# Performance work log

Measured on AMD Instinct MI355X. Metric: run time of the kernel, lower is better.

The kernel has to match this reference:

```python
import jax, jax.numpy as jnp
import numpy as np

N_AGENTS = 8; N_HEADS = 4; HYP = 128; EMB = 32; ENT_DIM = 64
BS = 64; T = 64; NE = 32


def setup_inputs() -> dict:
    key = jax.random.key(0)
    ks = jax.random.split(key, 8)
    p = lambda k, shape: jax.random.normal(k, shape, dtype=jnp.float32) * 0.1
    return {
        "agent_qs": jax.random.normal(ks[0], (BS, T, N_AGENTS), dtype=jnp.float32),
        "entities": jax.random.normal(ks[1], (BS, T, NE, ENT_DIM), dtype=jnp.float32),
        "entity_mask": jax.random.randint(ks[2], (BS, T, NE), 0, 2, dtype=jnp.int32),
        "fc1_w": p(ks[3], (4, HYP, ENT_DIM)), "fc1_b": jnp.zeros((4, HYP), jnp.float32),
        "qkv_w": p(ks[4], (4, 3 * HYP, HYP)), "qkv_b": jnp.zeros((4, 3 * HYP), jnp.float32),
        "out_w": p(ks[5], (4, HYP, HYP)), "out_b": jnp.zeros((4, HYP), jnp.float32),
        "fc2_w": p(ks[6], (4, EMB, HYP)), "fc2_b": jnp.zeros((4, EMB), jnp.float32),
    }


def _hypernet(entities, emask, fc1_w, fc1_b, qkv_w, qkv_b, out_w, out_b, fc2_w, fc2_b):
    # entities: [B, ne, ed]; emask: [B, ne] int (1 = entity absent)
    B, ne, _ = entities.shape
    hd = HYP // N_HEADS
    x1 = jax.nn.relu(jnp.einsum('bne,he->bnh', entities, fc1_w) + fc1_b)  # [B, ne, HYP]
    agent_mask = emask[:, :N_AGENTS]                                      # [B, na]
    # attn_mask = 1 - (1-agent_mask) x (1-entity_mask); nonzero => masked out
    attn_mask = 1.0 - (1.0 - agent_mask.astype(jnp.float32))[:, :, None] * \
                      (1.0 - emask.astype(jnp.float32))[:, None, :]       # [B, na, ne]
    qkv = jnp.einsum('bnh,gh->bng', x1, qkv_w) + qkv_b                    # [B, ne, 3*HYP]
    q, k, v = jnp.split(qkv, 3, axis=-1)
    q = q[:, :N_AGENTS].reshape(B, N_AGENTS, N_HEADS, hd).transpose(0, 2, 1, 3)
    k = k.reshape(B, ne, N_HEADS, hd).transpose(0, 2, 1, 3)
    v = v.reshape(B, ne, N_HEADS, hd).transpose(0, 2, 1, 3)
    logits = jnp.einsum('bhqd,bhkd->bhqk', q, k) / jnp.sqrt(jnp.float32(hd))
    masked = attn_mask[:, None] > 0                                       # [B, 1, na, ne]
    logits = jnp.where(masked, -1e9, logits)
    w = jax.nn.softmax(logits, axis=-1)
    # rows fully masked -> zero weights (matches nan-fill in torch impl)
    w = jnp.where(jnp.all(masked, axis=-1, keepdims=True), 0.0, w)
    attn = jnp.einsum('bhqk,bhkd->bhqd', w, v).transpose(0, 2, 1, 3).reshape(B, N_AGENTS, HYP)
    x2 = jnp.einsum('bnh,oh->bno', attn, out_w) + out_b
    x2 = jnp.where(agent_mask[:, :, None] > 0, 0.0, x2)                   # post_mask
    x3 = jnp.einsum('bnh,eh->bne', x2, fc2_w) + fc2_b
    x3 = jnp.where(agent_mask[:, :, None] > 0, 0.0, x3)                   # masked_fill
    return x3  # [B, n_agents, EMB]


def reference(agent_qs, entities, entity_mask, fc1_w, fc1_b, qkv_w, qkv_b, out_w, out_b, fc2_w, fc2_b):
    bs, t, ne, ed = entities.shape
    ents = entities.reshape(bs * t, ne, ed)
    emask = entity_mask.reshape(bs * t, ne)
    qs = agent_qs.reshape(bs * t, 1, N_AGENTS)
    # vmap over the 4 stacked hypernets (w1, b1, w_final, V)
    outs = jax.vmap(_hypernet, in_axes=(None, None, 0, 0, 0, 0, 0, 0, 0, 0))(
        ents, emask, fc1_w, fc1_b, qkv_w, qkv_b, out_w, out_b, fc2_w, fc2_b)
    w1 = jax.nn.softmax(outs[0], axis=-1)            # matrix mode: [B, na, EMB]
    b1 = outs[1].mean(axis=1)[:, None, :]            # vector mode: [B, 1, EMB]
    wf = outs[2].mean(axis=1)[:, :, None]            # vector mode: [B, EMB, 1]
    wf = jax.nn.softmax(wf, axis=-1)                 # softmax over size-1 dim (faithful)
    v = outs[3].mean(axis=(1, 2))[:, None, None]     # scalar mode: [B, 1, 1]
    hidden = jnp.einsum('bqa,bae->bqe', qs, w1) + b1
    y = jnp.einsum('bqe,bek->bqk', hidden, wf) + v
    return y.reshape(bs, t, 1)
```

## Files before the change

kernel.cpp:

```cpp
#include <hip/hip_runtime.h>
#include <math.h>

#define BPB 4
#define NBLK 1024
#define SCALE 0.17677669529663687f

typedef short short8 __attribute__((ext_vector_type(8)));
typedef float f32x4 __attribute__((ext_vector_type(4)));

__device__ __forceinline__ unsigned short f2bf(float x) {
  unsigned int u = __float_as_uint(x);
  u += 0x7fffu + ((u >> 16) & 1u);
  return (unsigned short)(u >> 16);
}
__device__ __forceinline__ unsigned pk2(float a, float b) {
  return (unsigned)f2bf(a) | ((unsigned)f2bf(b) << 16);
}
__device__ __forceinline__ float bf2f(unsigned int lo16) {
  return __uint_as_float(lo16 << 16);
}
__device__ __forceinline__ int tile_addr(int r, int k) {
  int g = k >> 3;
  int p = (g ^ ((r >> 1) & 3)) & 3;
  return r * 32 + p * 8 + (k & 7);
}
__device__ __forceinline__ int rm_addr(int r, int k) {
  int g = k >> 3;
  int r3 = r & 7;
  int rot = ((r3 << 2) | (r3 >> 1)) & 7;
  int p = (g & 8) | ((g & 7) ^ rot);
  return r * 128 + p * 8 + (k & 7);
}

__global__ void prep(const float* __restrict__ fc1_w, const float* __restrict__ qkv_w,
                     const float* __restrict__ qkv_b, const float* __restrict__ out_w,
                     const float* __restrict__ out_b, const float* __restrict__ fc2_w,
                     const float* __restrict__ fc2_b,
                     unsigned short* __restrict__ wbf, float* __restrict__ wsf) {
  const int blk = blockIdx.x;
  const int t = threadIdx.x;
  __shared__ float cw[128], ow2[128], red[128];
  if (blk < 40) {
    int o = blk * 256 + t;
    const float* src;
    int dst;
    if (o < 2048) {
      int gi = o >> 10, rem = o & 1023, n = rem >> 3, kg = rem & 7;
      int g = gi ? 3 : 1;
      src = fc1_w + ((g << 7) + n) * 64 + kg * 8;
      int lane = (kg & 3) * 16 + (n & 15);
      int f = (n >> 4) * 2 + (kg >> 2);
      dst = ((gi * 16 + f) * 64 + lane) * 8;
    } else if (o < 6144) {
      int o2 = o - 2048;
      int gi = o2 >> 11, rem = o2 & 2047, n = rem >> 4, kg = rem & 15;
      int g = gi ? 3 : 1;
      src = qkv_w + ((g * 384 + 128 + n) << 7) + kg * 8;
      int lane = (kg & 3) * 16 + (n & 15);
      int f = (n >> 4) * 4 + (kg >> 2);
      dst = 16384 + ((gi * 32 + f) * 64 + lane) * 8;
    } else {
      int o2 = o - 6144;
      int gi = o2 >> 11, rem = o2 & 2047, n = rem >> 4, kg = rem & 15;
      int g = gi ? 3 : 1;
      src = qkv_w + ((g * 384 + n) << 7) + kg * 8;
      int lane = (kg & 3) * 16 + (n & 15);
      int f = (n >> 4) * 4 + (kg >> 2);
      dst = 49152 + ((gi * 32 + f) * 64 + lane) * 8;
    }
    float4 v0 = *(const float4*)src;
    float4 v1 = *(const float4*)(src + 4);
    uint4 p;
    p.x = pk2(v0.x, v0.y); p.y = pk2(v0.z, v0.w);
    p.z = pk2(v1.x, v1.y); p.w = pk2(v1.z, v1.w);
    *(uint4*)&wbf[dst] = p;
  } else {
    const int gi = blk - 40;
    const int g = gi ? 3 : 1;
    if (t < 128) {
      const float* fw = fc2_w + g * 32 * 128;
      float s = 0.f;
      for (int e = 0; e < 32; ++e) s += fw[e * 128 + t];
      cw[t] = s;
    }
    __syncthreads();
    if (t < 128) {
      const float* ow = out_w + g * 128 * 128;
      float s = 0.f;
      for (int h = 0; h < 128; ++h) s += ow[h * 128 + t] * cw[h];
      ow2[t] = s;
    }
    __syncthreads();
    float* wsg = wsf + gi * 1024;
    const float* qwv = qkv_w + (size_t)(g * 3 + 2) * 128 * 128;
    for (int o = t; o < 512; o += 256) {
      int hh = o >> 7, h2 = o & 127;
      float s = 0.f;
      for (int d = 0; d < 32; ++d) s += qwv[(hh * 32 + d) * 128 + h2] * ow2[hh * 32 + d];
      wsg[o] = s;
    }
    if (t < 4) {
      const float* qbv = qkv_b + g * 384 + 256;
      float s = 0.f;
      for (int d = 0; d < 32; ++d) s += qbv[t * 32 + d] * ow2[t * 32 + d];
      wsg[512 + t] = s;
    }
    if (t < 128) {
      float x = out_b[g * 128 + t] * cw[t];
      if (t < 32) x += fc2_b[g * 32 + t];
      red[t] = x;
    }
    __syncthreads();
    if (t < 64) {
      float s = red[t] + red[t + 64];
      for (int o = 32; o; o >>= 1) s += __shfl_xor(s, o, 64);
      if (t == 0) wsg[516] = s;
    }
  }
}

__global__ __launch_bounds__(512, 4)
void mixer(const float* __restrict__ agent_qs,
           const float* __restrict__ entities,
           const int* __restrict__ emask,
           const float* __restrict__ fc1_b,
           const float* __restrict__ qkv_b,
           const unsigned short* __restrict__ wbf,
           const float* __restrict__ wsf,
           float* __restrict__ out) {
  __shared__ __align__(16) unsigned short sEK[16384];
  __shared__ __align__(16) unsigned short sX1[16384];
  __shared__ __align__(16) unsigned short sQ[4096];
  __shared__ __align__(16) float sVW[1024];
  __shared__ float sVP[BPB][4][32];
  __shared__ int sMm[128];
  __shared__ float sS[8];

  const int t = threadIdx.x;
  const int lane = t & 63;
  const int w = t >> 6;
  const int r = lane & 15, kg = lane >> 4;
  const int bb0 = blockIdx.x * BPB;

  if (t < 128) sMm[t] = emask[bb0 * 32 + t];

  const short8* W1f = (const short8*)wbf;
  const short8* Wkf = (const short8*)(wbf + 16384);
  const short8* Wqf = (const short8*)(wbf + 49152);

  float wreg[4][2][4];

  for (int gi = 0; gi < 2; ++gi) {
    const int g = gi ? 3 : 1;
    {
      const float4* Eg = (const float4*)entities + (size_t)bb0 * 512;
#pragma unroll
      for (int i = 0; i < 4; ++i) {
        int f4 = i * 512 + t;
        float4 v = Eg[f4];
        int k4 = f4 & 15, e = (f4 >> 4) & 31, bbi = f4 >> 9;
        int k = k4 * 4;
        int addr = bbi * 2048 + ((e >> 4) * 2 + (k >> 5)) * 512 + tile_addr(e & 15, k & 31);
        uint2 pkv;
        pkv.x = pk2(v.x, v.y);
        pkv.y = pk2(v.z, v.w);
        *(uint2*)&sEK[addr] = pkv;
      }
      if (t < 256) ((float4*)sVW)[t] = ((const float4*)(wsf + gi * 1024))[t];
    }
    __syncthreads();
    {
      const int b = w >> 1, mtl = w & 1;
      f32x4 acc[8];
#pragma unroll
      for (int nt = 0; nt < 8; ++nt) acc[nt] = {0.f, 0.f, 0.f, 0.f};
#pragma unroll
      for (int kc = 0; kc < 2; ++kc) {
        short8 ef = *(const short8*)&sEK[b * 2048 + (mtl * 2 + kc) * 512 + tile_addr(r, kg * 8)];
#pragma unroll
        for (int nt = 0; nt < 8; ++nt)
          acc[nt] = __builtin_amdgcn_mfma_f32_16x16x32_bf16(
              W1f[(gi * 16 + nt * 2 + kc) * 64 + lane], ef, acc[nt], 0, 0, 0);
      }
      const float* b1 = fc1_b + g * 128;
#pragma unroll
      for (int nt = 0; nt < 8; ++nt) {
        int hbase = nt * 16 + kg * 4;
        float4 bb4 = *(const float4*)&b1[hbase];
        float v0 = fmaxf(acc[nt][0] + bb4.x, 0.f);
        float v1 = fmaxf(acc[nt][1] + bb4.y, 0.f);
        float v2 = fmaxf(acc[nt][2] + bb4.z, 0.f);
        float v3 = fmaxf(acc[nt][3] + bb4.w, 0.f);
        uint2 pkv;
        pkv.x = pk2(v0, v1);
        pkv.y = pk2(v2, v3);
        *(uint2*)&sX1[b * 4096 + (mtl * 4 + (hbase >> 5)) * 512 + tile_addr(r, hbase & 31)] = pkv;
      }
    }
    __syncthreads();
    {
      const int b = w >> 1, mtl = w & 1;
      f32x4 acc[8];
#pragma unroll
      for (int nt = 0; nt < 8; ++nt) acc[nt] = {0.f, 0.f, 0.f, 0.f};
#pragma unroll
      for (int kc = 0; kc < 4; ++kc) {
        short8 xf = *(const short8*)&sX1[b * 4096 + (mtl * 4 + kc) * 512 + tile_addr(r, kg * 8)];
#pragma unroll
        for (int nt = 0; nt < 8; ++nt)
          acc[nt] = __builtin_amdgcn_mfma_f32_16x16x32_bf16(
              Wkf[(gi * 32 + nt * 4 + kc) * 64 + lane], xf, acc[nt], 0, 0, 0);
      }
      const float* bk = qkv_b + g * 384 + 128;
      const int ent = mtl * 16 + r;
#pragma unroll
      for (int nt = 0; nt < 8; ++nt) {
        int hbase = nt * 16 + kg * 4;
        float4 bb4 = *(const float4*)&bk[hbase];
        uint2 pkv;
        pkv.x = pk2(acc[nt][0] + bb4.x, acc[nt][1] + bb4.y);
        pkv.y = pk2(acc[nt][2] + bb4.z, acc[nt][3] + bb4.w);
        *(uint2*)&sEK[b * 4096 + rm_addr(ent, hbase)] = pkv;
      }
      const int mt = w >> 2, ntp = w & 3;
      const int b_rd = mt * 2 + (r >> 3);
      f32x4 qacc[2];
      qacc[0] = {0.f, 0.f, 0.f, 0.f};
      qacc[1] = {0.f, 0.f, 0.f, 0.f};
#pragma unroll
      for (int kc = 0; kc < 4; ++kc) {
        short8 xf = *(const short8*)&sX1[b_rd * 4096 + kc * 512 + tile_addr(r & 7, kg * 8)];
#pragma unroll
        for (int j = 0; j < 2; ++j)
          qacc[j] = __builtin_amdgcn_mfma_f32_16x16x32_bf16(
              Wqf[(gi * 32 + (ntp * 2 + j) * 4 + kc) * 64 + lane], xf, qacc[j], 0, 0, 0);
      }
      const float* bq = qkv_b + g * 384;
#pragma unroll
      for (int j = 0; j < 2; ++j) {
        int hbase = (ntp * 2 + j) * 16 + kg * 4;
        float4 bb4 = *(const float4*)&bq[hbase];
        uint2 pkv;
        pkv.x = pk2(qacc[j][0] + bb4.x, qacc[j][1] + bb4.y);
        pkv.y = pk2(qacc[j][2] + bb4.z, qacc[j][3] + bb4.w);
        *(uint2*)&sQ[(mt * 2 + (r >> 3)) * 1024 + rm_addr(r & 7, hbase)] = pkv;
      }
      const int vb = w >> 1;
      const int e = lane & 31;
      const int hh = (w & 1) * 2 + (lane >> 5);
      const int emt = e >> 4, er = e & 15;
      float a0 = sVW[512 + hh];
#pragma unroll
      for (int kc = 0; kc < 4; ++kc) {
#pragma unroll
        for (int gg = 0; gg < 4; ++gg) {
          uint4 u = *(const uint4*)&sX1[vb * 4096 + (emt * 4 + kc) * 512 + tile_addr(er, gg * 8)];
          const float* wv = &sVW[hh * 128 + kc * 32 + gg * 8];
          a0 = fmaf(bf2f(u.x & 0xffffu), wv[0], a0);
          a0 = fmaf(bf2f(u.x >> 16), wv[1], a0);
          a0 = fmaf(bf2f(u.y & 0xffffu), wv[2], a0);
          a0 = fmaf(bf2f(u.y >> 16), wv[3], a0);
          a0 = fmaf(bf2f(u.z & 0xffffu), wv[4], a0);
          a0 = fmaf(bf2f(u.z >> 16), wv[5], a0);
          a0 = fmaf(bf2f(u.w & 0xffffu), wv[6], a0);
          a0 = fmaf(bf2f(u.w >> 16), wv[7], a0);
        }
      }
      sVP[vb][hh][e] = a0;
    }
    __syncthreads();
    if (w < 4) {
      const int b = w;
      const int cl = r;
      bool ea0 = (sMm[b * 32 + cl] == 0);
      bool ea1 = (sMm[b * 32 + 16 + cl] == 0);
      bool aa[4];
#pragma unroll
      for (int reg = 0; reg < 4; ++reg) aa[reg] = (sMm[b * 32 + ((kg * 4 + reg) & 7)] == 0);
#pragma unroll
      for (int hh = 0; hh < 4; ++hh) {
        short8 af = *(const short8*)&sQ[b * 1024 + rm_addr(lane & 7, hh * 32 + kg * 8)];
        f32x4 z = {0.f, 0.f, 0.f, 0.f};
        short8 bf0 = *(const short8*)&sEK[b * 4096 + rm_addr(cl, hh * 32 + kg * 8)];
        f32x4 d0 = __builtin_amdgcn_mfma_f32_16x16x32_bf16(af, bf0, z, 0, 0, 0);
        short8 bf1 = *(const short8*)&sEK[b * 4096 + rm_addr(16 + cl, hh * 32 + kg * 8)];
        f32x4 d1 = __builtin_amdgcn_mfma_f32_16x16x32_bf16(af, bf1, z, 0, 0, 0);
#pragma unroll
        for (int reg = 0; reg < 4; ++reg) {
          float lg0 = (ea0 && aa[reg]) ? d0[reg] * SCALE : -1e30f;
          float lg1 = (ea1 && aa[reg]) ? d1[reg] * SCALE : -1e30f;
          float m = fmaxf(lg0, lg1);
          for (int o = 8; o; o >>= 1) m = fmaxf(m, __shfl_xor(m, o, 16));
          float p0 = lg0 > -1e29f ? __expf(lg0 - m) : 0.f;
          float p1 = lg1 > -1e29f ? __expf(lg1 - m) : 0.f;
          float s = p0 + p1;
          for (int o = 8; o; o >>= 1) s += __shfl_xor(s, o, 16);
          float inv = s > 0.f ? 1.f / s : 0.f;
          wreg[hh][0][reg] = p0 * inv;
          wreg[hh][1][reg] = p1 * inv;
        }
      }
      float c = 0.f;
#pragma unroll
      for (int hh = 0; hh < 4; ++hh) {
        float vp0 = sVP[b][hh][cl];
        float vp1 = sVP[b][hh][16 + cl];
        float s0 = wreg[hh][0][0] + wreg[hh][0][1] + wreg[hh][0][2] + wreg[hh][0][3];
        float s1 = wreg[hh][1][0] + wreg[hh][1][1] + wreg[hh][1][2] + wreg[hh][1][3];
        c = fmaf(vp0, s0, fmaf(vp1, s1, c));
      }
      for (int o = 16; o; o >>= 1) c += __shfl_xor(c, o, 32);
      if (lane == 0) {
        int cnt = 0;
        for (int a = 0; a < 8; ++a) cnt += (sMm[b * 32 + a] == 0);
        sS[gi * 4 + b] = c + sVW[516] * (float)cnt;
      }
    }
    __syncthreads();
  }

  if (t < BPB) {
    const float4* qs = (const float4*)(agent_qs + (size_t)(bb0 + t) * 8);
    float4 a = qs[0], b4 = qs[1];
    float q = a.x + a.y + a.z + a.w + b4.x + b4.y + b4.z + b4.w;
    out[bb0 + t] = q + sS[t] * 0.125f + sS[4 + t] * (1.f / 256.f);
  }
}

extern "C" void kernel_launch(void* const* d_in, const int* in_sizes, int n_in,
                              void* d_out, int out_size, void* d_ws, size_t ws_size,
                              hipStream_t stream) {
  const float* agent_qs = (const float*)d_in[0];
  const float* entities = (const float*)d_in[1];
  const int* emask = (const int*)d_in[2];
  const float* fc1_w = (const float*)d_in[3];
  const float* fc1_b = (const float*)d_in[4];
  const float* qkv_w = (const float*)d_in[5];
  const float* qkv_b = (const float*)d_in[6];
  const float* out_w = (const float*)d_in[7];
  const float* out_b = (const float*)d_in[8];
  const float* fc2_w = (const float*)d_in[9];
  const float* fc2_b = (const float*)d_in[10];
  float* out = (float*)d_out;
  unsigned short* wbf = (unsigned short*)d_ws;
  float* wsf = (float*)((char*)d_ws + 163840);

  prep<<<42, 256, 0, stream>>>(fc1_w, qkv_w, qkv_b, out_w, out_b, fc2_w, fc2_b, wbf, wsf);
  mixer<<<NBLK, 512, 0, stream>>>(agent_qs, entities, emask, fc1_b, qkv_b, wbf, wsf, out);
}
```

Baseline: 174.6 us.

## Fold V-projection into K MFMA tile and halve per-block batch

The collapsed value-projection vectors are packed as an extra bf16 MFMA N-tile next to the K weights, so the per-entity V reduction is done with MFMA instead of a scalar FMA loop over bf16 LDS reads. The prep kernel is split across more blocks and writes these rows plus zero padding. The mixer now handles 2 batch rows per 256-thread block instead of 4 per 512, with separate LDS buffers for E and K so entities are converted once rather than per hypernet. The V path now uses bf16 weights, which lowers its precision, and the block size and occupancy change.

```diff
diff --git a/kernel.cpp b/kernel.cpp
--- a/kernel.cpp
+++ b/kernel.cpp
@@ -1,12 +1,13 @@
 #include <hip/hip_runtime.h>
 #include <math.h>
 
-#define BPB 4
-#define NBLK 1024
+#define BPB 2
+#define NBLK 2048
 #define SCALE 0.17677669529663687f
 
 typedef short short8 __attribute__((ext_vector_type(8)));
 typedef float f32x4 __attribute__((ext_vector_type(4)));
+typedef unsigned short ushort_t;
 
 __device__ __forceinline__ unsigned short f2bf(float x) {
   unsigned int u = __float_as_uint(x);
@@ -15,9 +16,6 @@
 }
 __device__ __forceinline__ unsigned pk2(float a, float b) {
   return (unsigned)f2bf(a) | ((unsigned)f2bf(b) << 16);
-}
-__device__ __forceinline__ float bf2f(unsigned int lo16) {
-  return __uint_as_float(lo16 << 16);
 }
 __device__ __forceinline__ int tile_addr(int r, int k) {
   int g = k >> 3;
@@ -39,7 +37,7 @@
                      unsigned short* __restrict__ wbf, float* __restrict__ wsf) {
   const int blk = blockIdx.x;
   const int t = threadIdx.x;
-  __shared__ float cw[128], ow2[128], red[128];
+  __shared__ float cw[128], red[256], ow2s[32];
   if (blk < 40) {
     int o = blk * 256 + t;
     const float* src;
@@ -58,7 +56,7 @@
       src = qkv_w + ((g * 384 + 128 + n) << 7) + kg * 8;
       int lane = (kg & 3) * 16 + (n & 15);
       int f = (n >> 4) * 4 + (kg >> 2);
-      dst = 16384 + ((gi * 32 + f) * 64 + lane) * 8;
+      dst = 16384 + ((gi * 36 + f) * 64 + lane) * 8;
     } else {
       int o2 = o - 6144;
       int gi = o2 >> 11, rem = o2 & 2047, n = rem >> 4, kg = rem & 15;
@@ -66,7 +64,7 @@
       src = qkv_w + ((g * 384 + n) << 7) + kg * 8;
       int lane = (kg & 3) * 16 + (n & 15);
       int f = (n >> 4) * 4 + (kg >> 2);
-      dst = 49152 + ((gi * 32 + f) * 64 + lane) * 8;
+      dst = 53248 + ((gi * 32 + f) * 64 + lane) * 8;
     }
     float4 v0 = *(const float4*)src;
     float4 v1 = *(const float4*)(src + 4);
@@ -75,51 +73,72 @@
     p.z = pk2(v1.x, v1.y); p.w = pk2(v1.z, v1.w);
     *(uint4*)&wbf[dst] = p;
   } else {
-    const int gi = blk - 40;
+    const int mb = blk - 40;
+    const int gi = mb >> 2, hh = mb & 3;
     const int g = gi ? 3 : 1;
+    {
+      const float* fw = fc2_w + g * 4096;
+      int h2 = t & 127, half = t >> 7;
+      float s = 0.f;
+      for (int e = half * 16; e < half * 16 + 16; ++e) s += fw[e * 128 + h2];
+      red[t] = s;
+    }
+    __syncthreads();
+    if (t < 128) cw[t] = red[t] + red[t + 128];
+    __syncthreads();
+    {
+      const float* ow = out_w + g * 16384;
+      int hp = hh * 32 + (t & 31), ch = t >> 5;
+      float s = 0.f;
+      for (int h = ch * 16; h < ch * 16 + 16; ++h) s += ow[h * 128 + hp] * cw[h];
+      red[t] = s;
+    }
+    __syncthreads();
+    if (t < 32) {
+      float s = 0.f;
+      for (int c = 0; c < 8; ++c) s += red[c * 32 + t];
+      ow2s[t] = s;
+    }
+    __syncthreads();
+    {
+      const float* qwv = qkv_w + (size_t)(g * 3 + 2) * 16384;
+      int h2 = t & 127, half = t >> 7;
+      float s = 0.f;
+      for (int d = half * 16; d < half * 16 + 16; ++d)
+        s += qwv[(hh * 32 + d) * 128 + h2] * ow2s[d];
+      red[t] = s;
+    }
+    __syncthreads();
     if (t < 128) {
-      const float* fw = fc2_w + g * 32 * 128;
-      float s = 0.f;
-      for (int e = 0; e < 32; ++e) s += fw[e * 128 + t];
-      cw[t] = s;
-    }
-    __syncthreads();
-    if (t < 128) {
-      const float* ow = out_w + g * 128 * 128;
-      float s = 0.f;
-      for (int h = 0; h < 128; ++h) s += ow[h * 128 + t] * cw[h];
-      ow2[t] = s;
-    }
-    __syncthreads();
-    float* wsg = wsf + gi * 1024;
-    const float* qwv = qkv_w + (size_t)(g * 3 + 2) * 128 * 128;
-    for (int o = t; o < 512; o += 256) {
-      int hh = o >> 7, h2 = o & 127;
-      float s = 0.f;
-      for (int d = 0; d < 32; ++d) s += qwv[(hh * 32 + d) * 128 + h2] * ow2[hh * 32 + d];
-      wsg[o] = s;
-    }
-    if (t < 4) {
-      const float* qbv = qkv_b + g * 384 + 256;
-      float s = 0.f;
-      for (int d = 0; d < 32; ++d) s += qbv[t * 32 + d] * ow2[t * 32 + d];
-      wsg[512 + t] = s;
-    }
-    if (t < 128) {
-      float x = out_b[g * 128 + t] * cw[t];
-      if (t < 32) x += fc2_b[g * 32 + t];
-      red[t] = x;
-    }
-    __syncthreads();
-    if (t < 64) {
-      float s = red[t] + red[t + 64];
-      for (int o = 32; o; o >>= 1) s += __shfl_xor(s, o, 64);
-      if (t == 0) wsg[516] = s;
+      float v = red[t] + red[t + 128];
+      int k = t, kc = k >> 5, kg2 = k >> 3, j = k & 7;
+      wbf[16384 + ((gi * 36 + 32 + kc) * 64 + ((kg2 & 3) * 16 + hh)) * 8 + j] = f2bf(v);
+    }
+    if (t < 32) red[t] = qkv_b[g * 384 + 256 + hh * 32 + t] * ow2s[t];
+    __syncthreads();
+    if (t < 32) {
+      float s = red[t];
+      for (int o = 16; o; o >>= 1) s += __shfl_xor(s, o, 32);
+      if (t == 0) wsf[gi * 1024 + 512 + hh] = s;
+    }
+    if (hh == 0) {
+      for (int idx = t; idx < 1536; idx += 256) {
+        int n = 4 + (idx >> 7), k = idx & 127;
+        int kc = k >> 5, kg2 = k >> 3, j = k & 7;
+        wbf[16384 + ((gi * 36 + 32 + kc) * 64 + ((kg2 & 3) * 16 + n)) * 8 + j] = 0;
+      }
+      if (t < 128) red[t] = out_b[g * 128 + t] * cw[t] + (t < 32 ? fc2_b[g * 32 + t] : 0.f);
+      __syncthreads();
+      if (t < 64) {
+        float s = red[t] + red[t + 64];
+        for (int o = 32; o; o >>= 1) s += __shfl_xor(s, o, 64);
+        if (t == 0) wsf[gi * 1024 + 516] = s;
+      }
     }
   }
 }
 
-__global__ __launch_bounds__(512, 4)
+__global__ __launch_bounds__(256, 3)
 void mixer(const float* __restrict__ agent_qs,
            const float* __restrict__ entities,
            const int* __restrict__ emask,
@@ -128,13 +147,13 @@
            const unsigned short* __restrict__ wbf,
            const float* __restrict__ wsf,
            float* __restrict__ out) {
-  __shared__ __align__(16) unsigned short sEK[16384];
-  __shared__ __align__(16) unsigned short sX1[16384];
-  __shared__ __align__(16) unsigned short sQ[4096];
-  __shared__ __align__(16) float sVW[1024];
+  __shared__ __align__(16) ushort_t sE[4096];
+  __shared__ __align__(16) ushort_t sX1[8192];
+  __shared__ __align__(16) ushort_t sK[8192];
+  __shared__ __align__(16) ushort_t sQ[2048];
   __shared__ float sVP[BPB][4][32];
-  __shared__ int sMm[128];
-  __shared__ float sS[8];
+  __shared__ int sMm[64];
+  __shared__ float sS[4];
 
   const int t = threadIdx.x;
   const int lane = t & 63;
@@ -142,41 +161,41 @@
   const int r = lane & 15, kg = lane >> 4;
   const int bb0 = blockIdx.x * BPB;
 
-  if (t < 128) sMm[t] = emask[bb0 * 32 + t];
+  if (t < 64) sMm[t] = emask[bb0 * 32 + t];
 
   const short8* W1f = (const short8*)wbf;
-  const short8* Wkf = (const short8*)(wbf + 16384);
-  const short8* Wqf = (const short8*)(wbf + 49152);
+  const short8* Wkvf = (const short8*)(wbf + 16384);
+  const short8* Wqf = (const short8*)(wbf + 53248);
+
+  {
+    const float4* Eg = (const float4*)entities + (size_t)bb0 * 512;
+#pragma unroll
+    for (int i = 0; i < 4; ++i) {
+      int f4 = i * 256 + t;
+      float4 v = Eg[f4];
+      int k4 = f4 & 15, e = (f4 >> 4) & 31, bbi = f4 >> 9;
+      int k = k4 * 4;
+      int addr = bbi * 2048 + ((e >> 4) * 2 + (k >> 5)) * 512 + tile_addr(e & 15, k & 31);
+      uint2 pkv;
+      pkv.x = pk2(v.x, v.y);
+      pkv.y = pk2(v.z, v.w);
+      *(uint2*)&sE[addr] = pkv;
+    }
+  }
+  __syncthreads();
 
   float wreg[4][2][4];
 
   for (int gi = 0; gi < 2; ++gi) {
     const int g = gi ? 3 : 1;
     {
-      const float4* Eg = (const float4*)entities + (size_t)bb0 * 512;
-#pragma unroll
-      for (int i = 0; i < 4; ++i) {
-        int f4 = i * 512 + t;
-        float4 v = Eg[f4];
-        int k4 = f4 & 15, e = (f4 >> 4) & 31, bbi = f4 >> 9;
-        int k = k4 * 4;
-        int addr = bbi * 2048 + ((e >> 4) * 2 + (k >> 5)) * 512 + tile_addr(e & 15, k & 31);
-        uint2 pkv;
-        pkv.x = pk2(v.x, v.y);
-        pkv.y = pk2(v.z, v.w);
-        *(uint2*)&sEK[addr] = pkv;
-      }
-      if (t < 256) ((float4*)sVW)[t] = ((const float4*)(wsf + gi * 1024))[t];
-    }
-    __syncthreads();
-    {
       const int b = w >> 1, mtl = w & 1;
       f32x4 acc[8];
 #pragma unroll
       for (int nt = 0; nt < 8; ++nt) acc[nt] = {0.f, 0.f, 0.f, 0.f};
 #pragma unroll
       for (int kc = 0; kc < 2; ++kc) {
-        short8 ef = *(const short8*)&sEK[b * 2048 + (mtl * 2 + kc) * 512 + tile_addr(r, kg * 8)];
+        short8 ef = *(const short8*)&sE[b * 2048 + (mtl * 2 + kc) * 512 + tile_addr(r, kg * 8)];
 #pragma unroll
         for (int nt = 0; nt < 8; ++nt)
           acc[nt] = __builtin_amdgcn_mfma_f32_16x16x32_bf16(
@@ -200,16 +219,16 @@
     __syncthreads();
     {
       const int b = w >> 1, mtl = w & 1;
-      f32x4 acc[8];
-#pragma unroll
-      for (int nt = 0; nt < 8; ++nt) acc[nt] = {0.f, 0.f, 0.f, 0.f};
+      f32x4 acc[9];
+#pragma unroll
+      for (int nt = 0; nt < 9; ++nt) acc[nt] = {0.f, 0.f, 0.f, 0.f};
 #pragma unroll
       for (int kc = 0; kc < 4; ++kc) {
         short8 xf = *(const short8*)&sX1[b * 4096 + (mtl * 4 + kc) * 512 + tile_addr(r, kg * 8)];
 #pragma unroll
-        for (int nt = 0; nt < 8; ++nt)
+        for (int nt = 0; nt < 9; ++nt)
           acc[nt] = __builtin_amdgcn_mfma_f32_16x16x32_bf16(
-              Wkf[(gi * 32 + nt * 4 + kc) * 64 + lane], xf, acc[nt], 0, 0, 0);
+              Wkvf[(gi * 36 + nt * 4 + kc) * 64 + lane], xf, acc[nt], 0, 0, 0);
       }
       const float* bk = qkv_b + g * 384 + 128;
       const int ent = mtl * 16 + r;
@@ -220,56 +239,38 @@
         uint2 pkv;
         pkv.x = pk2(acc[nt][0] + bb4.x, acc[nt][1] + bb4.y);
         pkv.y = pk2(acc[nt][2] + bb4.z, acc[nt][3] + bb4.w);
-        *(uint2*)&sEK[b * 4096 + rm_addr(ent, hbase)] = pkv;
-      }
-      const int mt = w >> 2, ntp = w & 3;
-      const int b_rd = mt * 2 + (r >> 3);
+        *(uint2*)&sK[b * 4096 + rm_addr(ent, hbase)] = pkv;
+      }
+      if (kg == 0) {
+#pragma unroll
+        for (int reg = 0; reg < 4; ++reg)
+          sVP[b][reg][ent] = acc[8][reg] + wsf[gi * 1024 + 512 + reg];
+      }
       f32x4 qacc[2];
       qacc[0] = {0.f, 0.f, 0.f, 0.f};
       qacc[1] = {0.f, 0.f, 0.f, 0.f};
+      const int b_rd = r >> 3;
 #pragma unroll
       for (int kc = 0; kc < 4; ++kc) {
         short8 xf = *(const short8*)&sX1[b_rd * 4096 + kc * 512 + tile_addr(r & 7, kg * 8)];
 #pragma unroll
         for (int j = 0; j < 2; ++j)
           qacc[j] = __builtin_amdgcn_mfma_f32_16x16x32_bf16(
-              Wqf[(gi * 32 + (ntp * 2 + j) * 4 + kc) * 64 + lane], xf, qacc[j], 0, 0, 0);
+              Wqf[(gi * 32 + (w * 2 + j) * 4 + kc) * 64 + lane], xf, qacc[j], 0, 0, 0);
       }
       const float* bq = qkv_b + g * 384;
 #pragma unroll
       for (int j = 0; j < 2; ++j) {
-        int hbase = (ntp * 2 + j) * 16 + kg * 4;
+        int hbase = (w * 2 + j) * 16 + kg * 4;
         float4 bb4 = *(const float4*)&bq[hbase];
         uint2 pkv;
         pkv.x = pk2(qacc[j][0] + bb4.x, qacc[j][1] + bb4.y);
         pkv.y = pk2(qacc[j][2] + bb4.z, qacc[j][3] + bb4.w);
-        *(uint2*)&sQ[(mt * 2 + (r >> 3)) * 1024 + rm_addr(r & 7, hbase)] = pkv;
-      }
-      const int vb = w >> 1;
-      const int e = lane & 31;
-      const int hh = (w & 1) * 2 + (lane >> 5);
-      const int emt = e >> 4, er = e & 15;
-      float a0 = sVW[512 + hh];
-#pragma unroll
-      for (int kc = 0; kc < 4; ++kc) {
-#pragma unroll
-        for (int gg = 0; gg < 4; ++gg) {
-          uint4 u = *(const uint4*)&sX1[vb * 4096 + (emt * 4 + kc) * 512 + tile_addr(er, gg * 8)];
-          const float* wv = &sVW[hh * 128 + kc * 32 + gg * 8];
-          a0 = fmaf(bf2f(u.x & 0xffffu), wv[0], a0);
-          a0 = fmaf(bf2f(u.x >> 16), wv[1], a0);
-          a0 = fmaf(bf2f(u.y & 0xffffu), wv[2], a0);
-          a0 = fmaf(bf2f(u.y >> 16), wv[3], a0);
-          a0 = fmaf(bf2f(u.z & 0xffffu), wv[4], a0);
-          a0 = fmaf(bf2f(u.z >> 16), wv[5], a0);
-          a0 = fmaf(bf2f(u.w & 0xffffu), wv[6], a0);
-          a0 = fmaf(bf2f(u.w >> 16), wv[7], a0);
-        }
-      }
-      sVP[vb][hh][e] = a0;
-    }
-    __syncthreads();
-    if (w < 4) {
+        *(uint2*)&sQ[(r >> 3) * 1024 + rm_addr(r & 7, hbase)] = pkv;
+      }
+    }
+    __syncthreads();
+    if (w < BPB) {
       const int b = w;
       const int cl = r;
       bool ea0 = (sMm[b * 32 + cl] == 0);
@@ -281,9 +282,9 @@
       for (int hh = 0; hh < 4; ++hh) {
         short8 af = *(const short8*)&sQ[b * 1024 + rm_addr(lane & 7, hh * 32 + kg * 8)];
         f32x4 z = {0.f, 0.f, 0.f, 0.f};
-        short8 bf0 = *(const short8*)&sEK[b * 4096 + rm_addr(cl, hh * 32 + kg * 8)];
+        short8 bf0 = *(const short8*)&sK[b * 4096 + rm_addr(cl, hh * 32 + kg * 8)];
         f32x4 d0 = __builtin_amdgcn_mfma_f32_16x16x32_bf16(af, bf0, z, 0, 0, 0);
-        short8 bf1 = *(const short8*)&sEK[b * 4096 + rm_addr(16 + cl, hh * 32 + kg * 8)];
+        short8 bf1 = *(const short8*)&sK[b * 4096 + rm_addr(16 + cl, hh * 32 + kg * 8)];
         f32x4 d1 = __builtin_amdgcn_mfma_f32_16x16x32_bf16(af, bf1, z, 0, 0, 0);
 #pragma unroll
         for (int reg = 0; reg < 4; ++reg) {
@@ -313,7 +314,7 @@
       if (lane == 0) {
         int cnt = 0;
         for (int a = 0; a < 8; ++a) cnt += (sMm[b * 32 + a] == 0);
-        sS[gi * 4 + b] = c + sVW[516] * (float)cnt;
+        sS[gi * 2 + b] = c + wsf[gi * 1024 + 516] * (float)cnt;
       }
     }
     __syncthreads();
@@ -323,7 +324,7 @@
     const float4* qs = (const float4*)(agent_qs + (size_t)(bb0 + t) * 8);
     float4 a = qs[0], b4 = qs[1];
     float q = a.x + a.y + a.z + a.w + b4.x + b4.y + b4.z + b4.w;
-    out[bb0 + t] = q + sS[t] * 0.125f + sS[4 + t] * (1.f / 256.f);
+    out[bb0 + t] = q + sS[t] * 0.125f + sS[2 + t] * (1.f / 256.f);
   }
 }
 
@@ -343,8 +344,8 @@
   const float* fc2_b = (const float*)d_in[10];
   float* out = (float*)d_out;
   unsigned short* wbf = (unsigned short*)d_ws;
-  float* wsf = (float*)((char*)d_ws + 163840);
-
-  prep<<<42, 256, 0, stream>>>(fc1_w, qkv_w, qkv_b, out_w, out_b, fc2_w, fc2_b, wbf, wsf);
-  mixer<<<NBLK, 512, 0, stream>>>(agent_qs, entities, emask, fc1_b, qkv_b, wbf, wsf, out);
-}
+  float* wsf = (float*)((char*)d_ws + 172032);
+
+  prep<<<48, 256, 0, stream>>>(fc1_w, qkv_w, qkv_b, out_w, out_b, fc2_w, fc2_b, wbf, wsf);
+  mixer<<<NBLK, 256, 0, stream>>>(agent_qs, entities, emask, fc1_b, qkv_b, wbf, wsf, out);
+}
```

Result: faster. 151.9 us (-13.0%).
